# Performance work log

Hardware: AMD Instinct MI355X
Metric: run time of the kernel (lower is better)

## Reference

```python
import jax, jax.numpy as jnp
import numpy as np

D_MODEL = 1024
NUM_HEADS = 16
D_K = D_MODEL // NUM_HEADS


def setup_inputs() -> dict:
    key = jax.random.key(0)
    ks = jax.random.split(key, 11)
    B, S = 2, 2048
    s = 1.0 / np.sqrt(D_MODEL)
    return {
        "q": jax.random.normal(ks[0], (B, S, D_MODEL), jnp.float32),
        "k": jax.random.normal(ks[1], (B, S, D_MODEL), jnp.float32),
        "v": jax.random.normal(ks[2], (B, S, D_MODEL), jnp.float32),
        "w_q": jax.random.normal(ks[3], (D_MODEL, D_MODEL), jnp.float32) * s,
        "b_q": jnp.zeros((D_MODEL,), jnp.float32),
        "w_k": jax.random.normal(ks[4], (D_MODEL, D_MODEL), jnp.float32) * s,
        "b_k": jnp.zeros((D_MODEL,), jnp.float32),
        "w_v": jax.random.normal(ks[5], (D_MODEL, D_MODEL), jnp.float32) * s,
        "b_v": jnp.zeros((D_MODEL,), jnp.float32),
        "w_o": jax.random.normal(ks[6], (D_MODEL, D_MODEL), jnp.float32) * s,
        "b_o": jnp.zeros((D_MODEL,), jnp.float32),
    }


def reference(q, k, v, w_q, b_q, w_k, b_k, w_v, b_v, w_o, b_o):
    B, S, _ = q.shape
    H, Dk = NUM_HEADS, D_K

    def split_heads(x):  # [B,S,D] -> [B,H,S,Dk]
        return x.reshape(B, S, H, Dk).transpose(0, 2, 1, 3)

    # torch nn.Linear: x @ W.T + b
    qh = split_heads(q @ w_q.T + b_q)
    kh = split_heads(k @ w_k.T + b_k)
    vh = split_heads(v @ w_v.T + b_v)

    scale = 1.0 / jnp.sqrt(jnp.asarray(Dk, qh.dtype))
    scores = jnp.einsum("bhsd,bhtd->bhst", qh, kh) * scale  # [B,H,S,S]
    attn = jax.nn.softmax(scores, axis=-1)
    # dropout is identity in eval/deterministic baseline
    out = jnp.einsum("bhst,bhtd->bhsd", attn, vh)  # [B,H,S,Dk]
    out = out.transpose(0, 2, 1, 3).reshape(B, S, H * Dk)
    return out @ w_o.T + b_o
```

## Files before the change

### kernel.cpp

```cpp
#include <hip/hip_runtime.h>
#include <hip/hip_bf16.h>
#include <stdint.h>

typedef unsigned short u16;
typedef __attribute__((ext_vector_type(8))) short short8;
typedef __attribute__((ext_vector_type(8))) __bf16 bf16x8;
typedef __attribute__((ext_vector_type(4))) float f32x4;
typedef __attribute__((ext_vector_type(4))) uint32_t u32x4;

#if defined(__has_builtin)
#if __has_builtin(__builtin_amdgcn_global_load_lds)
#define USE_GLLDS 1
#endif
#endif

#if defined(__has_builtin)
#if __has_builtin(__builtin_amdgcn_exp2f)
#define HAVE_EXP2_BUILTIN 1
#endif
#endif
__device__ __forceinline__ float fexp2(float x) {
#ifdef HAVE_EXP2_BUILTIN
  return __builtin_amdgcn_exp2f(x);
#else
  return exp2f(x);
#endif
}

__device__ __forceinline__ u16 f2bf(float f) {
  __hip_bfloat16 h = __float2bfloat16(f);
  return __builtin_bit_cast(u16, h);
}

__device__ __forceinline__ f32x4 mfma16(bf16x8 a, bf16x8 b, f32x4 c) {
  return __builtin_amdgcn_mfma_f32_16x16x32_bf16(a, b, c, 0, 0, 0);
}

#ifdef USE_GLLDS
__device__ __forceinline__ void async_cp16(const void* g, void* l) {
  __builtin_amdgcn_global_load_lds(
      (const __attribute__((address_space(1))) void*)g,
      (__attribute__((address_space(3))) void*)l, 16, 0, 0);
}
#endif

__global__ __launch_bounds__(256) void cvt_all(
    const float* __restrict__ q, const float* __restrict__ k,
    const float* __restrict__ v, const float* __restrict__ w0,
    const float* __restrict__ w1, const float* __restrict__ w2,
    const float* __restrict__ w3, u16* __restrict__ dst) {
  size_t i = ((size_t)blockIdx.x * 256 + threadIdx.x) * 8;
  const size_t M1 = 1u << 20;
  const float* s;
  size_t base;
  if (i < 4 * M1) { s = q; base = 0; }
  else if (i < 8 * M1) { s = k; base = 4 * M1; }
  else if (i < 12 * M1) { s = v; base = 8 * M1; }
  else if (i < 13 * M1) { s = w0; base = 12 * M1; }
  else if (i < 14 * M1) { s = w1; base = 13 * M1; }
  else if (i < 15 * M1) { s = w2; base = 14 * M1; }
  else { s = w3; base = 15 * M1; }
  const float4 a = *(const float4*)(s + (i - base));
  const float4 b = *(const float4*)(s + (i - base) + 4);
  short8 r;
  r[0] = (short)f2bf(a.x); r[1] = (short)f2bf(a.y);
  r[2] = (short)f2bf(a.z); r[3] = (short)f2bf(a.w);
  r[4] = (short)f2bf(b.x); r[5] = (short)f2bf(b.y);
  r[6] = (short)f2bf(b.z); r[7] = (short)f2bf(b.w);
  *(short8*)(dst + i) = r;
}

__device__ __forceinline__ void gemm_core(const u16* __restrict__ X,
                                          const u16* __restrict__ W,
                                          const float* __restrict__ bias,
                                          void* __restrict__ outp, int mode,
                                          int m0, int n0) {
  __shared__ u16 Al[2][128 * 64];
  __shared__ u16 Bl[2][128 * 64];
  const int tid = threadIdx.x;
  const int wv = tid >> 6, l = tid & 63;
  const int wr = wv >> 1, wc = wv & 1;
  const int lrow = l & 15, lk = (l >> 4) * 8;

  f32x4 acc[4][4];
#pragma unroll
  for (int i = 0; i < 4; ++i)
#pragma unroll
    for (int j = 0; j < 4; ++j) acc[i][j] = (f32x4){0.f, 0.f, 0.f, 0.f};

  const u16* Asrc = X + (size_t)(m0 + (tid >> 3)) * 1024 + (tid & 7) * 8;
  const u16* Bsrc = W + (size_t)(tid >> 3) * 1024 + (tid & 7) * 8;

#ifdef USE_GLLDS
#define GSTAGE(buf, kt)                                                       \
  do {                                                                        \
    _Pragma("unroll")                                                         \
    for (int p = 0; p < 4; ++p) {                                             \
      async_cp16(Asrc + (size_t)p * 32 * 1024 + (kt),                         \
                 &Al[buf][p * 2048 + wv * 512]);                              \
      async_cp16(Bsrc + (size_t)p * 32 * 1024 + (kt),                         \
                 &Bl[buf][p * 2048 + wv * 512]);                              \
    }                                                                         \
  } while (0)
#else
#define GSTAGE(buf, kt)                                                       \
  do {                                                                        \
    short8 ar_[4], br_[4];                                                    \
    _Pragma("unroll")                                                         \
    for (int p = 0; p < 4; ++p) {                                             \
      ar_[p] = *(const short8*)(Asrc + (size_t)p * 32 * 1024 + (kt));         \
      br_[p] = *(const short8*)(Bsrc + (size_t)p * 32 * 1024 + (kt));         \
    }                                                                         \
    _Pragma("unroll")                                                         \
    for (int p = 0; p < 4; ++p) {                                             \
      *(short8*)&Al[buf][p * 2048 + tid * 8] = ar_[p];                        \
      *(short8*)&Bl[buf][p * 2048 + tid * 8] = br_[p];                        \
    }                                                                         \
  } while (0)
#endif

  GSTAGE(0, 0);
  __syncthreads();

  for (int kt = 0; kt < 1024; kt += 64) {
    const int cur = (kt >> 6) & 1;
    if (kt < 1024 - 64) GSTAGE(cur ^ 1, kt + 64);
#pragma unroll
    for (int ks = 0; ks < 2; ++ks) {
      bf16x8 af[4], bf[4];
#pragma unroll
      for (int mf = 0; mf < 4; ++mf)
        af[mf] = *(const bf16x8*)&Al[cur][(wr * 64 + mf * 16 + lrow) * 64 +
                                         ks * 32 + lk];
#pragma unroll
      for (int nf = 0; nf < 4; ++nf)
        bf[nf] = *(const bf16x8*)&Bl[cur][(wc * 64 + nf * 16 + lrow) * 64 +
                                          ks * 32 + lk];
#pragma unroll
      for (int mf = 0; mf < 4; ++mf)
#pragma unroll
        for (int nf = 0; nf < 4; ++nf)
          acc[mf][nf] = mfma16(af[mf], bf[nf], acc[mf][nf]);
    }
    __syncthreads();
  }
#undef GSTAGE

  const int rb = (l >> 4) * 4;
#pragma unroll
  for (int mf = 0; mf < 4; ++mf) {
#pragma unroll
    for (int nf = 0; nf < 4; ++nf) {
      const int gn = n0 + wc * 64 + nf * 16 + lrow;
      const float bi = bias[gn];
#pragma unroll
      for (int r = 0; r < 4; ++r) {
        const int gm = m0 + wr * 64 + mf * 16 + rb + r;
        float val = acc[mf][nf][r] + bi;
        const int b = gm >> 11, s = gm & 2047, h = gn >> 6, d = gn & 63;
        if (mode == 3) {
          ((float*)outp)[(size_t)gm * 1024 + gn] = val;
        } else if (mode == 2) {
          ((u16*)outp)[(((size_t)((b * 16 + h) * 64 + d)) << 11) + s] = f2bf(val);
        } else {
          if (mode == 0) val *= 0.18033688f;
          ((u16*)outp)[(((size_t)((b * 16 + h) * 2048 + s)) << 6) + d] = f2bf(val);
        }
      }
    }
  }
}

__global__ __launch_bounds__(256, 2) void gemm_proj(
    const u16* __restrict__ qb, const u16* __restrict__ wqb,
    const float* __restrict__ b_q, const float* __restrict__ b_k,
    const float* __restrict__ b_v, u16* __restrict__ Qh) {
  const int s = blockIdx.x;
  const int xcd = s & 7, c = s >> 3;
  const int nx = (xcd >> 2) * 12 + (c % 12);
  const int my = (xcd & 3) * 8 + (c / 12);
  const int z = nx >> 3, nxl = nx & 7;
  const float* bias = (z == 0) ? b_q : ((z == 1) ? b_k : b_v);
  gemm_core(qb + ((size_t)z << 22), wqb + ((size_t)nx << 17), bias,
            Qh + ((size_t)z << 22), z, my * 128, nxl * 128);
}

__global__ __launch_bounds__(256, 2) void gemm_out(
    const u16* __restrict__ X, const u16* __restrict__ W,
    const float* __restrict__ bias, float* __restrict__ out) {
  const int s = blockIdx.x;
  const int xcd = s & 7, c = s >> 3;
  const int nx = (xcd >> 2) * 4 + (c & 3);
  const int my = (xcd & 3) * 8 + (c >> 2);
  gemm_core(X, W + ((size_t)nx << 17), bias, out, 3, my * 128, nx * 128);
}

__global__ __launch_bounds__(512, 4) void flash_attn4(
    const u16* __restrict__ Qh, const u16* __restrict__ Kh,
    const u16* __restrict__ VT, u16* __restrict__ Op,
    float2* __restrict__ ml) {
  __shared__ __align__(16) u16 Kbuf[4096];
  __shared__ __align__(16) u16 Vbuf[4096];
  __shared__ __align__(16) uint32_t Pl[8 * 576];

  const int tid = threadIdx.x;
  const int wv = tid >> 6, l = tid & 63;
  const int q = l & 15, g = l >> 4;

  const int s_lin = blockIdx.x + (blockIdx.y << 4) + (blockIdx.z << 9);
  const int o = ((s_lin & 7) << 7) + (s_lin >> 3);
  const int qt = o & 15, bh = (o >> 4) & 31, z = o >> 9;

  const u16* Qp = Qh + ((size_t)bh * 2048 + qt * 128 + wv * 16) * 64;
  const u16* Kp = Kh + (size_t)bh * 2048 * 64;
  const u16* Vp = VT + (size_t)bh * 64 * 2048;

  bf16x8 qf[2];
  qf[0] = *(const bf16x8*)(Qp + q * 64 + g * 8);
  qf[1] = *(const bf16x8*)(Qp + q * 64 + 32 + g * 8);

  f32x4 o_acc[4];
#pragma unroll
  for (int df = 0; df < 4; ++df) o_acc[df] = (f32x4){0.f, 0.f, 0.f, 0.f};
  float m = -1e30f, ls = 0.f;

  const int srow = l >> 3;
  const int scolq = (l & 7) ^ srow;
  const int pbase = wv * 576 + q * 36;
  const char* kb = (const char*)&Kbuf[0];
  const char* vb = (const char*)&Vbuf[0];
  const int rsw = (q & 7) << 4;

  const u16* kg = Kp + (size_t)(z * 1024 + wv * 8 + srow) * 64 + scolq * 8;
  const u16* vg = Vp + (size_t)(wv * 8 + srow) * 2048 + z * 1024 + scolq * 8;

  {
    short8 k0 = *(const short8*)kg;
    short8 v0 = *(const short8*)vg;
    *(short8*)&Kbuf[wv * 512 + l * 8] = k0;
    *(short8*)&Vbuf[wv * 512 + l * 8] = v0;
  }
  kg += 64 * 64;
  vg += 64;
  __syncthreads();

  for (int tt = 0; tt < 16; ++tt) {
    short8 kr, vr;
    if (tt < 15) {
      kr = *(const short8*)kg;
      vr = *(const short8*)vg;
      kg += 64 * 64;
      vg += 64;
    }

    f32x4 s[4];
#pragma unroll
    for (int nj = 0; nj < 4; ++nj) s[nj] = (f32x4){0.f, 0.f, 0.f, 0.f};
#pragma unroll
    for (int ks = 0; ks < 2; ++ks) {
#pragma unroll
      for (int nj = 0; nj < 4; ++nj) {
        bf16x8 kf = *(const bf16x8*)(kb + (nj * 16 + q) * 128 +
                                     (((ks * 4 + g) << 4) ^ rsw));
        s[nj] = mfma16(kf, qf[ks], s[nj]);
      }
    }

    const float a0 = fmaxf(fmaxf(s[0][0], s[0][1]), fmaxf(s[0][2], s[0][3]));
    const float a1 = fmaxf(fmaxf(s[1][0], s[1][1]), fmaxf(s[1][2], s[1][3]));
    const float a2 = fmaxf(fmaxf(s[2][0], s[2][1]), fmaxf(s[2][2], s[2][3]));
    const float a3 = fmaxf(fmaxf(s[3][0], s[3][1]), fmaxf(s[3][2], s[3][3]));
    float mt = fmaxf(fmaxf(a0, a1), fmaxf(a2, a3));
    mt = fmaxf(mt, __shfl_xor(mt, 16));
    mt = fmaxf(mt, __shfl_xor(mt, 32));
    if (!__all(mt <= m + 8.f)) {
      const float nm = fmaxf(m, mt);
      const float rf = fexp2(m - nm);
      m = nm;
      ls *= rf;
#pragma unroll
      for (int df = 0; df < 4; ++df) o_acc[df] *= rf;
    }
    float ps = 0.f;
#pragma unroll
    for (int nj = 0; nj < 4; ++nj)
#pragma unroll
      for (int r = 0; r < 4; ++r) {
        s[nj][r] = fexp2(s[nj][r] - m);
        ps += s[nj][r];
      }
    ps += __shfl_xor(ps, 16);
    ps += __shfl_xor(ps, 32);
    ls += ps;

#pragma unroll
    for (int nj = 0; nj < 4; ++nj)
#pragma unroll
      for (int pp = 0; pp < 2; ++pp) {
        uint32_t w = (uint32_t)f2bf(s[nj][2 * pp]) |
                     ((uint32_t)f2bf(s[nj][2 * pp + 1]) << 16);
        Pl[pbase + nj * 8 + g * 2 + pp] = w;
      }

#pragma unroll
    for (int ks = 0; ks < 2; ++ks) {
      u32x4 pw = *(const u32x4*)&Pl[pbase + ks * 16 + 4 * g];
      bf16x8 pf = __builtin_bit_cast(bf16x8, pw);
#pragma unroll
      for (int df = 0; df < 4; ++df) {
        bf16x8 vf = *(const bf16x8*)(vb + (df * 16 + q) * 128 +
                                     (((ks * 4 + g) << 4) ^ rsw));
        o_acc[df] = mfma16(vf, pf, o_acc[df]);
      }
    }

    __syncthreads();
    if (tt < 15) {
      *(short8*)&Kbuf[wv * 512 + l * 8] = kr;
      *(short8*)&Vbuf[wv * 512 + l * 8] = vr;
    }
    __syncthreads();
  }

  const float inv = 1.f / ls;
  const int rowb = qt * 128 + wv * 16 + q;
  const size_t prow = (size_t)(z * 32 + bh) * 2048 + rowb;
  u16* Po = Op + (prow << 6);
#pragma unroll
  for (int df = 0; df < 4; ++df)
#pragma unroll
    for (int pp = 0; pp < 2; ++pp) {
      uint32_t w = (uint32_t)f2bf(o_acc[df][2 * pp] * inv) |
                   ((uint32_t)f2bf(o_acc[df][2 * pp + 1] * inv) << 16);
      *(uint32_t*)(Po + df * 16 + 4 * g + 2 * pp) = w;
    }
  if (g == 0) ml[prow] = make_float2(m, ls);
}

__global__ __launch_bounds__(256) void combine(
    const uint32_t* __restrict__ Op32, const float2* __restrict__ ml,
    u16* __restrict__ AO) {
  const int j = blockIdx.x * 256 + threadIdx.x;
  const int rowid = j >> 5, w5 = j & 31;
  const float2 a = ml[rowid];
  const float2 c = ml[(1 << 16) + rowid];
  const float M = fmaxf(a.x, c.x);
  float w1 = a.y * fexp2(a.x - M);
  float w2 = c.y * fexp2(c.x - M);
  const float inv = 1.f / (w1 + w2);
  w1 *= inv;
  w2 *= inv;
  const uint32_t p1 = Op32[j];
  const uint32_t p2 = Op32[(1u << 21) + j];
  const float lo = w1 * __builtin_bit_cast(float, p1 << 16) +
                   w2 * __builtin_bit_cast(float, p2 << 16);
  const float hi = w1 * __builtin_bit_cast(float, p1 & 0xffff0000u) +
                   w2 * __builtin_bit_cast(float, p2 & 0xffff0000u);
  const uint32_t outw = (uint32_t)f2bf(lo) | ((uint32_t)f2bf(hi) << 16);
  const int bh = rowid >> 11, s = rowid & 2047, b = bh >> 4, h = bh & 15;
  ((uint32_t*)AO)[((size_t)(b * 2048 + s) << 9) + h * 32 + w5] = outw;
}

extern "C" void kernel_launch(void* const* d_in, const int* in_sizes, int n_in,
                              void* d_out, int out_size, void* d_ws,
                              size_t ws_size, hipStream_t stream) {
  const float* q = (const float*)d_in[0];
  const float* k = (const float*)d_in[1];
  const float* v = (const float*)d_in[2];
  const float* w_q = (const float*)d_in[3];
  const float* b_q = (const float*)d_in[4];
  const float* w_k = (const float*)d_in[5];
  const float* b_k = (const float*)d_in[6];
  const float* w_v = (const float*)d_in[7];
  const float* b_v = (const float*)d_in[8];
  const float* w_o = (const float*)d_in[9];
  const float* b_o = (const float*)d_in[10];

  u16* ws = (u16*)d_ws;
  u16* qb = ws;
  u16* wqb = ws + (12u << 20);
  u16* wob = ws + (15u << 20);
  u16* Qh = ws + (16u << 20);
  u16* Kh = ws + (20u << 20);
  u16* VT = ws + (24u << 20);
  u16* AO = ws + (28u << 20);
  u16* Op = ws;
  float2* ml = (float2*)(ws + (8u << 20));

  cvt_all<<<dim3(8192), dim3(256), 0, stream>>>(q, k, v, w_q, w_k, w_v, w_o, ws);
  gemm_proj<<<dim3(768), dim3(256), 0, stream>>>(qb, wqb, b_q, b_k, b_v, Qh);
  flash_attn4<<<dim3(16, 32, 2), dim3(512), 0, stream>>>(Qh, Kh, VT, Op, ml);
  combine<<<dim3(8192), dim3(256), 0, stream>>>((const uint32_t*)Op, ml, AO);
  gemm_out<<<dim3(256), dim3(256), 0, stream>>>(AO, wob, b_o, (float*)d_out);
}
```

Measured before the change: 164.8 us.

## Use 8-wave single-buffered GEMM tiles to raise occupancy in projection kernels

The shared GEMM core for the QKV and output projections now uses 512 threads (8 waves, each owning a 64x32 sub-tile) instead of 256 threads with 64x64 sub-tiles. Shared memory drops from a double buffer to a single buffer, and launch bounds rise to 6 blocks per CU. The aim is to hide global-load latency through more resident waves and lower per-wave register use, rather than through software double-buffering. In exchange, the prefetch/compute overlap inside a block is lost, since every k-step now waits on a barrier after its loads, and each wave does fewer MFMAs per LDS fragment read.

```diff
diff --git a/kernel.cpp b/kernel.cpp
--- a/kernel.cpp
+++ b/kernel.cpp
@@ -70,88 +70,72 @@
   *(short8*)(dst + i) = r;
 }
 
-__device__ __forceinline__ void gemm_core(const u16* __restrict__ X,
-                                          const u16* __restrict__ W,
-                                          const float* __restrict__ bias,
-                                          void* __restrict__ outp, int mode,
-                                          int m0, int n0) {
-  __shared__ u16 Al[2][128 * 64];
-  __shared__ u16 Bl[2][128 * 64];
+__device__ __forceinline__ void gemm_core8(const u16* __restrict__ X,
+                                           const u16* __restrict__ W,
+                                           const float* __restrict__ bias,
+                                           void* __restrict__ outp, int mode,
+                                           int m0, int n0) {
+  __shared__ u16 Al[128 * 64];
+  __shared__ u16 Bl[128 * 64];
   const int tid = threadIdx.x;
   const int wv = tid >> 6, l = tid & 63;
-  const int wr = wv >> 1, wc = wv & 1;
+  const int wr = wv >> 2, wc = wv & 3;
   const int lrow = l & 15, lk = (l >> 4) * 8;
 
-  f32x4 acc[4][4];
+  f32x4 acc[4][2];
 #pragma unroll
   for (int i = 0; i < 4; ++i)
 #pragma unroll
-    for (int j = 0; j < 4; ++j) acc[i][j] = (f32x4){0.f, 0.f, 0.f, 0.f};
-
-  const u16* Asrc = X + (size_t)(m0 + (tid >> 3)) * 1024 + (tid & 7) * 8;
-  const u16* Bsrc = W + (size_t)(tid >> 3) * 1024 + (tid & 7) * 8;
-
+    for (int j = 0; j < 2; ++j) acc[i][j] = (f32x4){0.f, 0.f, 0.f, 0.f};
+
+  const int srow = l >> 3;
+  const int scol = (l & 7) * 8;
+  const u16* Asrc = X + (size_t)(m0 + wv * 8 + srow) * 1024 + scol;
+  const u16* Bsrc = W + (size_t)(wv * 8 + srow) * 1024 + scol;
+
+  for (int kt = 0; kt < 1024; kt += 64) {
 #ifdef USE_GLLDS
-#define GSTAGE(buf, kt)                                                       \
-  do {                                                                        \
-    _Pragma("unroll")                                                         \
-    for (int p = 0; p < 4; ++p) {                                             \
-      async_cp16(Asrc + (size_t)p * 32 * 1024 + (kt),                         \
-                 &Al[buf][p * 2048 + wv * 512]);                              \
-      async_cp16(Bsrc + (size_t)p * 32 * 1024 + (kt),                         \
-                 &Bl[buf][p * 2048 + wv * 512]);                              \
-    }                                                                         \
-  } while (0)
+    async_cp16(Asrc + kt, &Al[(wv * 8) * 64]);
+    async_cp16(Asrc + (size_t)64 * 1024 + kt, &Al[(wv * 8 + 64) * 64]);
+    async_cp16(Bsrc + kt, &Bl[(wv * 8) * 64]);
+    async_cp16(Bsrc + (size_t)64 * 1024 + kt, &Bl[(wv * 8 + 64) * 64]);
 #else
-#define GSTAGE(buf, kt)                                                       \
-  do {                                                                        \
-    short8 ar_[4], br_[4];                                                    \
-    _Pragma("unroll")                                                         \
-    for (int p = 0; p < 4; ++p) {                                             \
-      ar_[p] = *(const short8*)(Asrc + (size_t)p * 32 * 1024 + (kt));         \
-      br_[p] = *(const short8*)(Bsrc + (size_t)p * 32 * 1024 + (kt));         \
-    }                                                                         \
-    _Pragma("unroll")                                                         \
-    for (int p = 0; p < 4; ++p) {                                             \
-      *(short8*)&Al[buf][p * 2048 + tid * 8] = ar_[p];                        \
-      *(short8*)&Bl[buf][p * 2048 + tid * 8] = br_[p];                        \
-    }                                                                         \
-  } while (0)
-#endif
-
-  GSTAGE(0, 0);
-  __syncthreads();
-
-  for (int kt = 0; kt < 1024; kt += 64) {
-    const int cur = (kt >> 6) & 1;
-    if (kt < 1024 - 64) GSTAGE(cur ^ 1, kt + 64);
+    short8 a0 = *(const short8*)(Asrc + kt);
+    short8 a1 = *(const short8*)(Asrc + (size_t)64 * 1024 + kt);
+    short8 b0 = *(const short8*)(Bsrc + kt);
+    short8 b1 = *(const short8*)(Bsrc + (size_t)64 * 1024 + kt);
+    *(short8*)&Al[(wv * 8 + srow) * 64 + scol] = a0;
+    *(short8*)&Al[(wv * 8 + 64 + srow) * 64 + scol] = a1;
+    *(short8*)&Bl[(wv * 8 + srow) * 64 + scol] = b0;
+    *(short8*)&Bl[(wv * 8 + 64 + srow) * 64 + scol] = b1;
+#endif
+    __syncthreads();
 #pragma unroll
     for (int ks = 0; ks < 2; ++ks) {
-      bf16x8 af[4], bf[4];
+      bf16x8 af[4], bf[2];
 #pragma unroll
       for (int mf = 0; mf < 4; ++mf)
-        af[mf] = *(const bf16x8*)&Al[cur][(wr * 64 + mf * 16 + lrow) * 64 +
-                                         ks * 32 + lk];
-#pragma unroll
-      for (int nf = 0; nf < 4; ++nf)
-        bf[nf] = *(const bf16x8*)&Bl[cur][(wc * 64 + nf * 16 + lrow) * 64 +
-                                          ks * 32 + lk];
+        af[mf] = *(const bf16x8*)&Al[(wr * 64 + mf * 16 + lrow) * 64 +
+                                     ks * 32 + lk];
+#pragma unroll
+      for (int nf = 0; nf < 2; ++nf)
+        bf[nf] = *(const bf16x8*)&Bl[(wc * 32 + nf * 16 + lrow) * 64 +
+                                     ks * 32 + lk];
 #pragma unroll
       for (int mf = 0; mf < 4; ++mf)
 #pragma unroll
-        for (int nf = 0; nf < 4; ++nf)
+        for (int nf = 0; nf < 2; ++nf)
           acc[mf][nf] = mfma16(af[mf], bf[nf], acc[mf][nf]);
     }
     __syncthreads();
   }
-#undef GSTAGE
 
   const int rb = (l >> 4) * 4;
 #pragma unroll
   for (int mf = 0; mf < 4; ++mf) {
 #pragma unroll
-    for (int nf = 0; nf < 4; ++nf) {
-      const int gn = n0 + wc * 64 + nf * 16 + lrow;
+    for (int nf = 0; nf < 2; ++nf) {
+      const int gn = n0 + wc * 32 + nf * 16 + lrow;
       const float bi = bias[gn];
 #pragma unroll
       for (int r = 0; r < 4; ++r) {
@@ -171,7 +155,7 @@
   }
 }
 
-__global__ __launch_bounds__(256, 2) void gemm_proj(
+__global__ __launch_bounds__(512, 6) void gemm_proj(
     const u16* __restrict__ qb, const u16* __restrict__ wqb,
     const float* __restrict__ b_q, const float* __restrict__ b_k,
     const float* __restrict__ b_v, u16* __restrict__ Qh) {
@@ -181,18 +165,18 @@
   const int my = (xcd & 3) * 8 + (c / 12);
   const int z = nx >> 3, nxl = nx & 7;
   const float* bias = (z == 0) ? b_q : ((z == 1) ? b_k : b_v);
-  gemm_core(qb + ((size_t)z << 22), wqb + ((size_t)nx << 17), bias,
-            Qh + ((size_t)z << 22), z, my * 128, nxl * 128);
-}
-
-__global__ __launch_bounds__(256, 2) void gemm_out(
+  gemm_core8(qb + ((size_t)z << 22), wqb + ((size_t)nx << 17), bias,
+             Qh + ((size_t)z << 22), z, my * 128, nxl * 128);
+}
+
+__global__ __launch_bounds__(512, 6) void gemm_out(
     const u16* __restrict__ X, const u16* __restrict__ W,
     const float* __restrict__ bias, float* __restrict__ out) {
   const int s = blockIdx.x;
   const int xcd = s & 7, c = s >> 3;
   const int nx = (xcd >> 2) * 4 + (c & 3);
   const int my = (xcd & 3) * 8 + (c >> 2);
-  gemm_core(X, W + ((size_t)nx << 17), bias, out, 3, my * 128, nx * 128);
+  gemm_core8(X, W + ((size_t)nx << 17), bias, out, 3, my * 128, nx * 128);
 }
 
 __global__ __launch_bounds__(512, 4) void flash_attn4(
@@ -388,8 +372,8 @@
   float2* ml = (float2*)(ws + (8u << 20));
 
   cvt_all<<<dim3(8192), dim3(256), 0, stream>>>(q, k, v, w_q, w_k, w_v, w_o, ws);
-  gemm_proj<<<dim3(768), dim3(256), 0, stream>>>(qb, wqb, b_q, b_k, b_v, Qh);
+  gemm_proj<<<dim3(768), dim3(512), 0, stream>>>(qb, wqb, b_q, b_k, b_v, Qh);
   flash_attn4<<<dim3(16, 32, 2), dim3(512), 0, stream>>>(Qh, Kh, VT, Op, ml);
   combine<<<dim3(8192), dim3(256), 0, stream>>>((const uint32_t*)Op, ml, AO);
-  gemm_out<<<dim3(256), dim3(256), 0, stream>>>(AO, wob, b_o, (float*)d_out);
-}
+  gemm_out<<<dim3(256), dim3(512), 0, stream>>>(AO, wob, b_o, (float*)d_out);
+}
```

Result: no change. 163.7 us (-0.7%).
